# Optimization experiments

Measured on AMD Instinct MI355X. Metric: run time of the kernel, lower is better.

The kernel has to match this reference:

```python
import jax, jax.numpy as jnp
import numpy as np

B, C, H, W = 4, 3, 1024, 1024
RADII = (8, 16, 32, 64)
EPS = 1e-5  # BatchNorm2d default eps


def _box_sum(x, r, s):
    # depthwise all-ones conv (kernel r, stride s, VALID padding) == summed box
    return jax.lax.reduce_window(x, 0.0, jax.lax.add, (1, 1, r, r), (1, 1, s, s), 'VALID')


def _axis_interp_ac(x, n_out, axis):
    # bilinear (align_corners=True) interpolation along one axis
    n_in = x.shape[axis]
    pos = jnp.arange(n_out, dtype=x.dtype) * ((n_in - 1) / max(n_out - 1, 1))
    i0 = jnp.clip(jnp.floor(pos).astype(jnp.int32), 0, n_in - 2)
    w = pos - i0.astype(x.dtype)
    a = jnp.take(x, i0, axis=axis)
    b = jnp.take(x, i0 + 1, axis=axis)
    shape = [1] * x.ndim
    shape[axis] = n_out
    w = w.reshape(shape)
    return a * (1 - w) + b * w


def _resize_ac(x, oh, ow):
    x = _axis_interp_ac(x, oh, 2)
    x = _axis_interp_ac(x, ow, 3)
    return x


def _bn(x, g, b, rm, rv):
    inv = g / jnp.sqrt(rv + EPS)
    return x * inv[None, :, None, None] + (b - rm * inv)[None, :, None, None]


def _forward(guide, src, w1, g1, b1, rm1, rv1, w2, g2, b2, rm2, rv2, w3):
    Hg, Wg = guide.shape[2], guide.shape[3]
    gg = guide * guide
    gs = guide * src
    ones = jnp.ones((1, guide.shape[1], Hg, Wg), guide.dtype)
    stats = []
    for r in RADII:
        s = r // 2
        N = _box_sum(ones, r, s)
        mx = _box_sum(guide, r, s) / N
        my = _box_sum(src, r, s) / N
        cov = _box_sum(gs, r, s) / N - mx * my
        var = _box_sum(gg, r, s) / N - mx * mx
        stats.append((mx, my, cov, var))
    mx1, my1, cov1, var1 = stats[0]
    oh, ow = cov1.shape[2], cov1.shape[3]
    feats = [cov1, var1]
    for (_, _, cov, var) in stats[1:]:
        feats.append(_resize_ac(cov, oh, ow))
        feats.append(_resize_ac(var, oh, ow))
    x = jnp.concatenate(feats, axis=1)  # [B,24,oh,ow]
    x = jax.nn.relu(_bn(jnp.einsum('oc,bchw->bohw', w1, x), g1, b1, rm1, rv1))
    x = jax.nn.relu(_bn(jnp.einsum('oc,bchw->bohw', w2, x), g2, b2, rm2, rv2))
    A = jnp.einsum('oc,bchw->bohw', w3, x)  # [B,3,oh,ow]
    bb = my1 - A * mx1
    mean_A = _resize_ac(A, Hg, Wg)
    mean_b = _resize_ac(bb, Hg, Wg)
    return mean_A * guide + mean_b


def setup_inputs() -> dict:
    key = jax.random.key(0)
    ks = jax.random.split(key, 5)
    f32 = jnp.float32
    return {
        'guide': jax.random.normal(ks[0], (B, C, H, W), f32),
        'src': jax.random.normal(ks[1], (B, C, H, W), f32),
        'w1': jax.random.normal(ks[2], (48, 24), f32) * 0.05,
        'g1': jnp.ones((48,), f32), 'b1': jnp.zeros((48,), f32),
        'rm1': jnp.zeros((48,), f32), 'rv1': jnp.ones((48,), f32),
        'w2': jax.random.normal(ks[3], (48, 48), f32) * 0.05,
        'g2': jnp.ones((48,), f32), 'b2': jnp.zeros((48,), f32),
        'rm2': jnp.zeros((48,), f32), 'rv2': jnp.ones((48,), f32),
        'w3': jax.random.normal(ks[4], (3, 48), f32) * 0.05,
    }


def reference(guide, src, w1, g1, b1, rm1, rv1, w2, g2, b2, rm2, rv2, w3):
    return _forward(guide, src, w1, g1, b1, rm1, rv1, w2, g2, b2, rm2, rv2, w3)
```

## Files before the change

kernel.cpp:

```cpp
#include <hip/hip_runtime.h>

#define HH 1024
#define WW 1024
#define NB 4
#define NC 3
#define BC 12
#define N1 255
#define N2 127
#define N3 63
#define N4 31
#define EPS 1e-5f

constexpr size_t S8_OFF  = 0;
constexpr size_t S8_SZ   = 4ull * BC * N1 * N1;
constexpr size_t S16_OFF = S8_OFF + S8_SZ;
constexpr size_t S16_SZ  = 4ull * BC * N2 * N2;
constexpr size_t S32_OFF = S16_OFF + S16_SZ;
constexpr size_t S32_SZ  = 4ull * BC * N3 * N3;
constexpr size_t S64_OFF = S32_OFF + S32_SZ;
constexpr size_t S64_SZ  = 4ull * BC * N4 * N4;
constexpr size_t CV16_OFF = S64_OFF + S64_SZ;
constexpr size_t CV16_SZ  = 2ull * BC * N2 * N2;
constexpr size_t CV32_OFF = CV16_OFF + CV16_SZ;
constexpr size_t CV32_SZ  = 2ull * BC * N3 * N3;
constexpr size_t CV64_OFF = CV32_OFF + CV32_SZ;
constexpr size_t CV64_SZ  = 2ull * BC * N4 * N4;
constexpr size_t A_OFF    = CV64_OFF + CV64_SZ;
constexpr size_t A_SZ     = (size_t)NB * NC * N1 * N1;
constexpr size_t BB_OFF   = A_OFF + A_SZ;
constexpr size_t WF_OFF   = BB_OFF + A_SZ;
constexpr int WF_W1 = 0;
constexpr int WF_B1 = 1152;
constexpr int WF_W2 = 1200;
constexpr int WF_B2 = 3504;
constexpr int WF_W3 = 3552;

__global__ __launch_bounds__(256) void prep_kernel(
    const float* __restrict__ w1, const float* __restrict__ g1,
    const float* __restrict__ b1, const float* __restrict__ rm1,
    const float* __restrict__ rv1,
    const float* __restrict__ w2, const float* __restrict__ g2,
    const float* __restrict__ b2, const float* __restrict__ rm2,
    const float* __restrict__ rv2,
    const float* __restrict__ w3, float* __restrict__ Wf)
{
    __shared__ float i1[48], i2[48];
    int t = threadIdx.x;
    if (t < 48) {
        float iv = g1[t] * rsqrtf(rv1[t] + EPS);
        i1[t] = iv;
        Wf[WF_B1 + t] = b1[t] - rm1[t] * iv;
        float iw = g2[t] * rsqrtf(rv2[t] + EPS);
        i2[t] = iw;
        Wf[WF_B2 + t] = b2[t] - rm2[t] * iw;
    }
    __syncthreads();
    for (int k = t; k < 48 * 24; k += 256) Wf[WF_W1 + k] = w1[k] * i1[k / 24];
    for (int k = t; k < 48 * 48; k += 256) Wf[WF_W2 + k] = w2[k] * i2[k / 48];
    for (int k = t; k < 3 * 48; k += 256)  Wf[WF_W3 + k] = w3[k];
}

__global__ __launch_bounds__(256) void base_kernel(
    const float* __restrict__ guide, const float* __restrict__ src,
    float* __restrict__ S8)
{
    int blk = blockIdx.x;
    int bc  = blk / N1;
    int i   = blk % N1;
    int j   = threadIdx.x;
    if (j >= N1) return;

    const float* g0 = guide + (size_t)bc * HH * WW + (size_t)(4 * i) * WW + 4 * j;
    const float* s0 = src   + (size_t)bc * HH * WW + (size_t)(4 * i) * WW + 4 * j;

    float sg = 0.f, ss = 0.f, sgg = 0.f, sgs = 0.f;
#pragma unroll
    for (int r = 0; r < 8; ++r) {
        float4 ga = *(const float4*)(g0 + (size_t)r * WW);
        float4 gb = *(const float4*)(g0 + (size_t)r * WW + 4);
        float4 sa = *(const float4*)(s0 + (size_t)r * WW);
        float4 sb = *(const float4*)(s0 + (size_t)r * WW + 4);
        float ge[8] = {ga.x, ga.y, ga.z, ga.w, gb.x, gb.y, gb.z, gb.w};
        float se[8] = {sa.x, sa.y, sa.z, sa.w, sb.x, sb.y, sb.z, sb.w};
#pragma unroll
        for (int k = 0; k < 8; ++k) {
            float g = ge[k], s = se[k];
            sg  += g;
            ss  += s;
            sgg += g * g;
            sgs += g * s;
        }
    }
    size_t qs  = (size_t)BC * N1 * N1;
    size_t idx = (size_t)bc * N1 * N1 + (size_t)i * N1 + j;
    S8[0 * qs + idx] = sg;
    S8[1 * qs + idx] = ss;
    S8[2 * qs + idx] = sgg;
    S8[3 * qs + idx] = sgs;
}

__global__ __launch_bounds__(256) void pyr_kernel(
    const float* __restrict__ Sin, float* __restrict__ Sout,
    float* __restrict__ CVout, int nin, int nout, float invN)
{
    int idx = blockIdx.x * blockDim.x + threadIdx.x;
    int total = BC * nout * nout;
    if (idx >= total) return;
    int j  = idx % nout;
    int t  = idx / nout;
    int i  = t % nout;
    int bc = t / nout;

    size_t sIn  = (size_t)BC * nin * nin;
    size_t base = (size_t)bc * nin * nin;
    int p = 2 * i, q = 2 * j;

    float sums[4];
#pragma unroll
    for (int qt = 0; qt < 4; ++qt) {
        const float* P = Sin + (size_t)qt * sIn + base;
        sums[qt] = P[(size_t)p * nin + q] + P[(size_t)(p + 2) * nin + q] +
                   P[(size_t)p * nin + q + 2] + P[(size_t)(p + 2) * nin + q + 2];
    }
    size_t sOut = (size_t)BC * nout * nout;
    size_t o    = (size_t)bc * nout * nout + (size_t)i * nout + j;
    Sout[0 * sOut + o] = sums[0];
    Sout[1 * sOut + o] = sums[1];
    Sout[2 * sOut + o] = sums[2];
    Sout[3 * sOut + o] = sums[3];
    float mx = sums[0] * invN, my = sums[1] * invN;
    CVout[o]        = sums[3] * invN - mx * my;
    CVout[sOut + o] = sums[2] * invN - mx * mx;
}

__global__ __launch_bounds__(256) void mlp_kernel(
    const float* __restrict__ S8,
    const float* __restrict__ CV16, const float* __restrict__ CV32,
    const float* __restrict__ CV64,
    const float* __restrict__ Wf,
    float* __restrict__ A, float* __restrict__ Bb)
{
    const float* __restrict__ W1 = Wf + WF_W1;
    const float* __restrict__ B1 = Wf + WF_B1;
    const float* __restrict__ W2 = Wf + WF_W2;
    const float* __restrict__ B2 = Wf + WF_B2;
    const float* __restrict__ W3 = Wf + WF_W3;

    int idx = blockIdx.x * 256 + threadIdx.x;
    if (idx >= NB * N1 * N1) return;
    int ox = idx % N1;
    int r  = idx / N1;
    int oy = r % N1;
    int b  = r / N1;

    float feats[24], mx1[3], my1[3];

    size_t s8q = (size_t)BC * N1 * N1;
    for (int c = 0; c < 3; ++c) {
        size_t o = (size_t)(b * 3 + c) * N1 * N1 + (size_t)oy * N1 + ox;
        float sg = S8[o], ss = S8[s8q + o], sgg = S8[2 * s8q + o], sgs = S8[3 * s8q + o];
        float mx = sg * (1.f / 64.f), my = ss * (1.f / 64.f);
        mx1[c] = mx; my1[c] = my;
        feats[c]     = sgs * (1.f / 64.f) - mx * my;
        feats[3 + c] = sgg * (1.f / 64.f) - mx * mx;
    }

    const float* CVs[3] = {CV16, CV32, CV64};
    const int nins[3]   = {N2, N3, N4};
    const float scales[3] = {(float)(126.0 / 254.0), (float)(62.0 / 254.0),
                             (float)(30.0 / 254.0)};
#pragma unroll
    for (int l = 0; l < 3; ++l) {
        const float* CV = CVs[l];
        int nin = nins[l];
        float sc = scales[l];
        float py = (float)oy * sc;
        int   i0 = min(max((int)floorf(py), 0), nin - 2);
        float wy = py - (float)i0;
        float px = (float)ox * sc;
        int   j0 = min(max((int)floorf(px), 0), nin - 2);
        float wx = px - (float)j0;
        size_t cvq = (size_t)BC * nin * nin;
        int fo = 6 + 6 * l;
        for (int c = 0; c < 3; ++c) {
            size_t bix = (size_t)(b * 3 + c) * nin * nin;
            size_t o00 = bix + (size_t)i0 * nin + j0;
            float c00 = CV[o00], c01 = CV[o00 + 1];
            float c10 = CV[o00 + nin], c11 = CV[o00 + nin + 1];
            feats[fo + c] = (c00 * (1.f - wy) + c10 * wy) * (1.f - wx) +
                            (c01 * (1.f - wy) + c11 * wy) * wx;
            float v00 = CV[cvq + o00], v01 = CV[cvq + o00 + 1];
            float v10 = CV[cvq + o00 + nin], v11 = CV[cvq + o00 + nin + 1];
            feats[fo + 3 + c] = (v00 * (1.f - wy) + v10 * wy) * (1.f - wx) +
                                (v01 * (1.f - wy) + v11 * wy) * wx;
        }
    }

    float h1[48];
#pragma unroll
    for (int o = 0; o < 48; ++o) {
        float acc = B1[o];
#pragma unroll
        for (int c = 0; c < 24; ++c) acc = fmaf(W1[o * 24 + c], feats[c], acc);
        h1[o] = fmaxf(acc, 0.f);
    }
    float h2[48];
#pragma unroll
    for (int o = 0; o < 48; ++o) {
        float acc = B2[o];
#pragma unroll
        for (int c = 0; c < 48; ++c) acc = fmaf(W2[o * 48 + c], h1[c], acc);
        h2[o] = fmaxf(acc, 0.f);
    }
#pragma unroll
    for (int c = 0; c < 3; ++c) {
        float acc = 0.f;
#pragma unroll
        for (int k = 0; k < 48; ++k) acc = fmaf(W3[c * 48 + k], h2[k], acc);
        size_t o = (size_t)(b * 3 + c) * N1 * N1 + (size_t)oy * N1 + ox;
        A[o]  = acc;
        Bb[o] = my1[c] - acc * mx1[c];
    }
}

__global__ __launch_bounds__(256) void final_kernel(
    const float* __restrict__ guide, const float* __restrict__ A,
    const float* __restrict__ Bb, float* __restrict__ out)
{
    __shared__ float aH[N1 + 1], bH[N1 + 1];
    int blk = blockIdx.x;
    int bc  = blk / HH;
    int h   = blk % HH;

    const float scale = (float)(254.0 / 1023.0);
    float py = (float)h * scale;
    int   i0 = min(max((int)floorf(py), 0), N1 - 2);
    float wy = py - (float)i0;

    int t = threadIdx.x;
    if (t < N1) {
        size_t base = (size_t)bc * N1 * N1 + (size_t)i0 * N1 + t;
        aH[t] = A[base] * (1.f - wy) + A[base + N1] * wy;
        bH[t] = Bb[base] * (1.f - wy) + Bb[base + N1] * wy;
    }
    __syncthreads();

    const float* gp = guide + (size_t)bc * HH * WW + (size_t)h * WW;
    float*       op = out   + (size_t)bc * HH * WW + (size_t)h * WW;

    float4 g4 = *(const float4*)(gp + 4 * t);
    float4 o4;
    float ge[4] = {g4.x, g4.y, g4.z, g4.w};
    float oe[4];
#pragma unroll
    for (int k = 0; k < 4; ++k) {
        int w = 4 * t + k;
        float px = (float)w * scale;
        int   j0 = min(max((int)floorf(px), 0), N1 - 2);
        float wx = px - (float)j0;
        float a = aH[j0] * (1.f - wx) + aH[j0 + 1] * wx;
        float bbv = bH[j0] * (1.f - wx) + bH[j0 + 1] * wx;
        oe[k] = a * ge[k] + bbv;
    }
    o4.x = oe[0]; o4.y = oe[1]; o4.z = oe[2]; o4.w = oe[3];
    *(float4*)(op + 4 * t) = o4;
}

extern "C" void kernel_launch(void* const* d_in, const int* in_sizes, int n_in,
                              void* d_out, int out_size, void* d_ws, size_t ws_size,
                              hipStream_t stream)
{
    const float* guide = (const float*)d_in[0];
    const float* src   = (const float*)d_in[1];
    const float* w1    = (const float*)d_in[2];
    const float* g1    = (const float*)d_in[3];
    const float* b1    = (const float*)d_in[4];
    const float* rm1   = (const float*)d_in[5];
    const float* rv1   = (const float*)d_in[6];
    const float* w2    = (const float*)d_in[7];
    const float* g2    = (const float*)d_in[8];
    const float* b2    = (const float*)d_in[9];
    const float* rm2   = (const float*)d_in[10];
    const float* rv2   = (const float*)d_in[11];
    const float* w3    = (const float*)d_in[12];
    float*       out   = (float*)d_out;

    float* ws   = (float*)d_ws;
    float* S8   = ws + S8_OFF;
    float* S16  = ws + S16_OFF;
    float* S32  = ws + S32_OFF;
    float* S64  = ws + S64_OFF;
    float* CV16 = ws + CV16_OFF;
    float* CV32 = ws + CV32_OFF;
    float* CV64 = ws + CV64_OFF;
    float* Abuf = ws + A_OFF;
    float* Bbuf = ws + BB_OFF;
    float* Wf   = ws + WF_OFF;

    prep_kernel<<<1, 256, 0, stream>>>(w1, g1, b1, rm1, rv1, w2, g2, b2, rm2, rv2,
                                       w3, Wf);

    base_kernel<<<BC * N1, 256, 0, stream>>>(guide, src, S8);

    {
        int total = BC * N2 * N2;
        pyr_kernel<<<(total + 255) / 256, 256, 0, stream>>>(S8, S16, CV16, N1, N2,
                                                            1.f / 256.f);
    }
    {
        int total = BC * N3 * N3;
        pyr_kernel<<<(total + 255) / 256, 256, 0, stream>>>(S16, S32, CV32, N2, N3,
                                                            1.f / 1024.f);
    }
    {
        int total = BC * N4 * N4;
        pyr_kernel<<<(total + 255) / 256, 256, 0, stream>>>(S32, S64, CV64, N3, N4,
                                                            1.f / 4096.f);
    }

    {
        int total = NB * N1 * N1;
        mlp_kernel<<<(total + 255) / 256, 256, 0, stream>>>(
            S8, CV16, CV32, CV64, Wf, Abuf, Bbuf);
    }

    final_kernel<<<BC * HH, 256, 0, stream>>>(guide, Abuf, Bbuf, out);
}
```

Baseline: 231.9 us.

## Reuse row sums across overlapping windows and fuse pyramid levels into one kernel

The base box-sum kernel now has each thread compute per-row partial sums over 20 input rows and accumulate them into four output rows. This cuts the redundant reads of overlapping 8x8 windows by about 2x. The weight-prep work moves into an extra block of the base kernel, and the three chained pyramid kernels become a single kernel that reads the S8 sums directly for every level. That removes launches and intermediate S16/S32/S64 writes, at the cost of more S8 reads for the coarser levels and fewer blocks in the base grid.

```diff
diff --git a/kernel.cpp b/kernel.cpp
--- a/kernel.cpp
+++ b/kernel.cpp
@@ -35,7 +35,9 @@
 constexpr int WF_B2 = 3504;
 constexpr int WF_W3 = 3552;
 
-__global__ __launch_bounds__(256) void prep_kernel(
+__global__ __launch_bounds__(256) void base_kernel(
+    const float* __restrict__ guide, const float* __restrict__ src,
+    float* __restrict__ S8,
     const float* __restrict__ w1, const float* __restrict__ g1,
     const float* __restrict__ b1, const float* __restrict__ rm1,
     const float* __restrict__ rv1,
@@ -45,92 +47,132 @@
     const float* __restrict__ w3, float* __restrict__ Wf)
 {
     __shared__ float i1[48], i2[48];
-    int t = threadIdx.x;
-    if (t < 48) {
-        float iv = g1[t] * rsqrtf(rv1[t] + EPS);
-        i1[t] = iv;
-        Wf[WF_B1 + t] = b1[t] - rm1[t] * iv;
-        float iw = g2[t] * rsqrtf(rv2[t] + EPS);
-        i2[t] = iw;
-        Wf[WF_B2 + t] = b2[t] - rm2[t] * iw;
-    }
-    __syncthreads();
-    for (int k = t; k < 48 * 24; k += 256) Wf[WF_W1 + k] = w1[k] * i1[k / 24];
-    for (int k = t; k < 48 * 48; k += 256) Wf[WF_W2 + k] = w2[k] * i2[k / 48];
-    for (int k = t; k < 3 * 48; k += 256)  Wf[WF_W3 + k] = w3[k];
-}
-
-__global__ __launch_bounds__(256) void base_kernel(
-    const float* __restrict__ guide, const float* __restrict__ src,
-    float* __restrict__ S8)
-{
     int blk = blockIdx.x;
-    int bc  = blk / N1;
-    int i   = blk % N1;
-    int j   = threadIdx.x;
+    int t   = threadIdx.x;
+
+    if (blk == BC * 64) {
+        if (t < 48) {
+            float iv = g1[t] * rsqrtf(rv1[t] + EPS);
+            i1[t] = iv;
+            Wf[WF_B1 + t] = b1[t] - rm1[t] * iv;
+            float iw = g2[t] * rsqrtf(rv2[t] + EPS);
+            i2[t] = iw;
+            Wf[WF_B2 + t] = b2[t] - rm2[t] * iw;
+        }
+        __syncthreads();
+        for (int k = t; k < 48 * 24; k += 256) Wf[WF_W1 + k] = w1[k] * i1[k / 24];
+        for (int k = t; k < 48 * 48; k += 256) Wf[WF_W2 + k] = w2[k] * i2[k / 48];
+        for (int k = t; k < 3 * 48; k += 256)  Wf[WF_W3 + k] = w3[k];
+        return;
+    }
+
+    int bc = blk / 64;
+    int i4 = blk % 64;
+    int j  = t;
     if (j >= N1) return;
 
-    const float* g0 = guide + (size_t)bc * HH * WW + (size_t)(4 * i) * WW + 4 * j;
-    const float* s0 = src   + (size_t)bc * HH * WW + (size_t)(4 * i) * WW + 4 * j;
-
-    float sg = 0.f, ss = 0.f, sgg = 0.f, sgs = 0.f;
-#pragma unroll
-    for (int r = 0; r < 8; ++r) {
-        float4 ga = *(const float4*)(g0 + (size_t)r * WW);
-        float4 gb = *(const float4*)(g0 + (size_t)r * WW + 4);
-        float4 sa = *(const float4*)(s0 + (size_t)r * WW);
-        float4 sb = *(const float4*)(s0 + (size_t)r * WW + 4);
+    int row0  = 16 * i4;
+    int nrows = (i4 == 63) ? 16 : 20;
+
+    const float* g0 = guide + (size_t)bc * HH * WW + (size_t)row0 * WW + 4 * j;
+    const float* s0 = src   + (size_t)bc * HH * WW + (size_t)row0 * WW + 4 * j;
+
+    float acc[4][4];
+#pragma unroll
+    for (int u = 0; u < 4; ++u)
+#pragma unroll
+        for (int q = 0; q < 4; ++q) acc[u][q] = 0.f;
+
+#pragma unroll
+    for (int rr = 0; rr < 20; ++rr) {
+        if (rr >= nrows) break;
+        float4 ga = *(const float4*)(g0 + (size_t)rr * WW);
+        float4 gb = *(const float4*)(g0 + (size_t)rr * WW + 4);
+        float4 sa = *(const float4*)(s0 + (size_t)rr * WW);
+        float4 sb = *(const float4*)(s0 + (size_t)rr * WW + 4);
         float ge[8] = {ga.x, ga.y, ga.z, ga.w, gb.x, gb.y, gb.z, gb.w};
         float se[8] = {sa.x, sa.y, sa.z, sa.w, sb.x, sb.y, sb.z, sb.w};
+        float rg = 0.f, rs = 0.f, rgg = 0.f, rgs = 0.f;
 #pragma unroll
         for (int k = 0; k < 8; ++k) {
             float g = ge[k], s = se[k];
-            sg  += g;
-            ss  += s;
-            sgg += g * g;
-            sgs += g * s;
-        }
-    }
-    size_t qs  = (size_t)BC * N1 * N1;
-    size_t idx = (size_t)bc * N1 * N1 + (size_t)i * N1 + j;
-    S8[0 * qs + idx] = sg;
-    S8[1 * qs + idx] = ss;
-    S8[2 * qs + idx] = sgg;
-    S8[3 * qs + idx] = sgs;
-}
-
-__global__ __launch_bounds__(256) void pyr_kernel(
-    const float* __restrict__ Sin, float* __restrict__ Sout,
-    float* __restrict__ CVout, int nin, int nout, float invN)
-{
-    int idx = blockIdx.x * blockDim.x + threadIdx.x;
-    int total = BC * nout * nout;
-    if (idx >= total) return;
-    int j  = idx % nout;
-    int t  = idx / nout;
-    int i  = t % nout;
-    int bc = t / nout;
-
-    size_t sIn  = (size_t)BC * nin * nin;
-    size_t base = (size_t)bc * nin * nin;
-    int p = 2 * i, q = 2 * j;
-
-    float sums[4];
-#pragma unroll
-    for (int qt = 0; qt < 4; ++qt) {
-        const float* P = Sin + (size_t)qt * sIn + base;
-        sums[qt] = P[(size_t)p * nin + q] + P[(size_t)(p + 2) * nin + q] +
-                   P[(size_t)p * nin + q + 2] + P[(size_t)(p + 2) * nin + q + 2];
-    }
-    size_t sOut = (size_t)BC * nout * nout;
-    size_t o    = (size_t)bc * nout * nout + (size_t)i * nout + j;
-    Sout[0 * sOut + o] = sums[0];
-    Sout[1 * sOut + o] = sums[1];
-    Sout[2 * sOut + o] = sums[2];
-    Sout[3 * sOut + o] = sums[3];
-    float mx = sums[0] * invN, my = sums[1] * invN;
-    CVout[o]        = sums[3] * invN - mx * my;
-    CVout[sOut + o] = sums[2] * invN - mx * mx;
+            rg  += g;
+            rs  += s;
+            rgg += g * g;
+            rgs += g * s;
+        }
+        const int ulo = (rr >= 7) ? ((rr - 4) >> 2) : 0;
+        const int uhi = ((rr >> 2) < 3) ? (rr >> 2) : 3;
+#pragma unroll
+        for (int u = ulo; u <= uhi; ++u) {
+            acc[u][0] += rg;
+            acc[u][1] += rs;
+            acc[u][2] += rgg;
+            acc[u][3] += rgs;
+        }
+    }
+
+    size_t qs = (size_t)BC * N1 * N1;
+#pragma unroll
+    for (int u = 0; u < 4; ++u) {
+        int orow = 4 * i4 + u;
+        if (orow <= N1 - 1) {
+            size_t idx = (size_t)bc * N1 * N1 + (size_t)orow * N1 + j;
+            S8[0 * qs + idx] = acc[u][0];
+            S8[1 * qs + idx] = acc[u][1];
+            S8[2 * qs + idx] = acc[u][2];
+            S8[3 * qs + idx] = acc[u][3];
+        }
+    }
+}
+
+__global__ __launch_bounds__(256) void pyrcv_kernel(
+    const float* __restrict__ S8,
+    float* __restrict__ CV16, float* __restrict__ CV32,
+    float* __restrict__ CV64)
+{
+    constexpr int T16 = BC * N2 * N2;
+    constexpr int T32 = BC * N3 * N3;
+    constexpr int T64 = BC * N4 * N4;
+
+    int idx = blockIdx.x * 256 + threadIdx.x;
+    int rem, ncell, nout;
+    float inv;
+    float* CV;
+    if (idx < T16) {
+        rem = idx; ncell = 2; nout = N2; inv = 1.f / 256.f; CV = CV16;
+    } else if (idx < T16 + T32) {
+        rem = idx - T16; ncell = 4; nout = N3; inv = 1.f / 1024.f; CV = CV32;
+    } else if (idx < T16 + T32 + T64) {
+        rem = idx - T16 - T32; ncell = 8; nout = N4; inv = 1.f / 4096.f; CV = CV64;
+    } else {
+        return;
+    }
+
+    int j  = rem % nout;
+    int tt = rem / nout;
+    int i  = tt % nout;
+    int bc = tt / nout;
+
+    size_t q8   = (size_t)BC * N1 * N1;
+    const float* base = S8 + (size_t)bc * N1 * N1;
+
+    float s0 = 0.f, s1 = 0.f, s2 = 0.f, s3 = 0.f;
+    for (int a = 0; a < ncell; ++a) {
+        size_t roff = (size_t)(ncell * i + 2 * a) * N1 + (size_t)(ncell * j);
+        for (int b = 0; b < ncell; ++b) {
+            size_t off = roff + 2 * b;
+            s0 += base[off];
+            s1 += base[q8 + off];
+            s2 += base[2 * q8 + off];
+            s3 += base[3 * q8 + off];
+        }
+    }
+    float mx = s0 * inv, my = s1 * inv;
+    size_t so = (size_t)BC * nout * nout;
+    size_t o  = (size_t)bc * nout * nout + (size_t)i * nout + j;
+    CV[o]      = s3 * inv - mx * my;
+    CV[so + o] = s2 * inv - mx * mx;
 }
 
 __global__ __launch_bounds__(256) void mlp_kernel(
@@ -287,9 +329,6 @@
 
     float* ws   = (float*)d_ws;
     float* S8   = ws + S8_OFF;
-    float* S16  = ws + S16_OFF;
-    float* S32  = ws + S32_OFF;
-    float* S64  = ws + S64_OFF;
     float* CV16 = ws + CV16_OFF;
     float* CV32 = ws + CV32_OFF;
     float* CV64 = ws + CV64_OFF;
@@ -297,25 +336,12 @@
     float* Bbuf = ws + BB_OFF;
     float* Wf   = ws + WF_OFF;
 
-    prep_kernel<<<1, 256, 0, stream>>>(w1, g1, b1, rm1, rv1, w2, g2, b2, rm2, rv2,
-                                       w3, Wf);
-
-    base_kernel<<<BC * N1, 256, 0, stream>>>(guide, src, S8);
+    base_kernel<<<BC * 64 + 1, 256, 0, stream>>>(
+        guide, src, S8, w1, g1, b1, rm1, rv1, w2, g2, b2, rm2, rv2, w3, Wf);
 
     {
-        int total = BC * N2 * N2;
-        pyr_kernel<<<(total + 255) / 256, 256, 0, stream>>>(S8, S16, CV16, N1, N2,
-                                                            1.f / 256.f);
-    }
-    {
-        int total = BC * N3 * N3;
-        pyr_kernel<<<(total + 255) / 256, 256, 0, stream>>>(S16, S32, CV32, N2, N3,
-                                                            1.f / 1024.f);
-    }
-    {
-        int total = BC * N4 * N4;
-        pyr_kernel<<<(total + 255) / 256, 256, 0, stream>>>(S32, S64, CV64, N3, N4,
-                                                            1.f / 4096.f);
+        constexpr int TOTAL = BC * (N2 * N2 + N3 * N3 + N4 * N4);
+        pyrcv_kernel<<<(TOTAL + 255) / 256, 256, 0, stream>>>(S8, CV16, CV32, CV64);
     }
 
     {
```

Result: slower. 245.8 us (+6.0%).
